# Kernel optimization log

Hardware: AMD Instinct MI355X
Metric: run time of the kernel (lower is better)

The kernel has to match this reference:

```python
import jax, jax.numpy as jnp
import numpy as np

ALPHA = 0.2  # LeakyReLU negative slope used throughout
NEG = -9e15


def _leaky(x, a=ALPHA):
    return jnp.where(x >= 0, x, a * x)


def _gat_layer(h, adj, W, a, concat):
    # h: [N, Fin], W: [Fin, Fout], a: [2*Fout, 1]
    Wh = h @ W                                   # [N, Fout]
    d = W.shape[-1]
    e = _leaky(Wh @ a[:d] + (Wh @ a[d:]).T)      # [N, N]
    att = jax.nn.softmax(jnp.where(adj > 0, e, NEG), axis=1)
    out = att @ Wh                               # [N, Fout]
    return jax.nn.elu(out) if concat else out


def setup_inputs() -> dict:
    key = jax.random.key(0)
    ks = jax.random.split(key, 24)
    N, F, H, D1, O1 = 4096, 512, 4, 256, 64
    x = jax.random.normal(ks[0], (N, F), dtype=jnp.float32)
    adj = jax.random.bernoulli(ks[1], 0.02, (N, N))
    adj = (adj | adj.T | jnp.eye(N, dtype=bool)).astype(jnp.float32)
    observation = jax.random.randint(ks[2], (1, N), 0, 2, dtype=jnp.int32)
    s_mat = jax.random.uniform(ks[3], (N, N), dtype=jnp.float32)
    theta = jax.random.uniform(ks[4], (1, F), dtype=jnp.float32)
    g = lambda k, s, sc: (jax.random.normal(k, s, dtype=jnp.float32) * sc)
    return {
        'x': x, 'adj': adj, 'observation': observation, 's_mat': s_mat,
        'theta': theta,
        'Wh0': g(ks[5], (H, F, D1), 0.05), 'ah0': g(ks[6], (H, 2 * D1, 1), 0.05),
        'Wh1': g(ks[7], (H, D1, D1), 0.05), 'ah1': g(ks[8], (H, 2 * D1, 1), 0.05),
        'Wo0': g(ks[9], (H * D1, O1), 0.05), 'ao0': g(ks[10], (2 * O1, 1), 0.05),
        'Wo1': g(ks[11], (O1, 1), 0.2), 'ao1': g(ks[12], (2, 1), 0.2),
        'dW': g(ks[13], (2, 10), 0.5), 'dW0': g(ks[14], (1, 10), 0.5),
        'dW1': g(ks[15], (10, 20), 0.5), 'dW01': g(ks[16], (1, 20), 0.5),
        'dW2': g(ks[17], (20, 10), 0.5), 'dW02': g(ks[18], (1, 10), 0.5),
        'dV': g(ks[19], (10, 1), 0.5), 'dV0': g(ks[20], (1, 1), 0.5),
    }


def reference(x, adj, observation, s_mat, theta, Wh0, ah0, Wh1, ah1,
              Wo0, ao0, Wo1, ao1, dW, dW0, dW1, dW01, dW2, dW02, dV, dV0):
    # mergeState: add theta to rows in the seed set (observation[0] == 1)
    seed = (observation[0] == 1).astype(x.dtype)[:, None]  # [N,1]
    h_in = x + seed * theta

    # multi-head 2-layer attention stacks (concat=True -> elu inside)
    def head(W0, a0, W1, a1):
        h = _gat_layer(h_in, adj, W0, a0, True)
        return _gat_layer(h, adj, W1, a1, True)

    hh = jax.vmap(head)(Wh0, ah0, Wh1, ah1)                 # [H, N, D1]
    hcat = jnp.transpose(hh, (1, 0, 2)).reshape(h_in.shape[0], -1)  # [N, H*D1]

    # output attention stack (concat=False), then elu (GAT.forward)
    h = _gat_layer(hcat, adj, Wo0, ao0, False)
    h = _gat_layer(h, adj, Wo1, ao1, False)
    h_ = jax.nn.elu(h)                                      # [N, 1]

    # GAT_degree v2: degreeNN over [h_, degree]
    d_v = s_mat.sum(axis=1, keepdims=True)                  # [N, 1]
    x_ = jnp.concatenate([h_, d_v], axis=1)                 # [N, 2]
    h0 = _leaky(x_ @ dW + dW0)
    h1 = _leaky(h0 @ dW1 + dW01)
    h2 = _leaky(h1 @ dW2 + dW02)
    return _leaky(h2 @ dV + dV0)                            # [N, 1]
```

## Files before the change

### kernel.cpp

```cpp
#include <hip/hip_runtime.h>
#include <hip/hip_bf16.h>
#include <hip/hip_fp16.h>
#include <math.h>

#define MAXDEG 512

typedef short v8s __attribute__((ext_vector_type(8)));
typedef float v4f __attribute__((ext_vector_type(4)));
typedef _Float16 h2 __attribute__((ext_vector_type(2)));

__device__ __forceinline__ float blockReduceSum(float v) {
    __shared__ float sh[8];
    int lane = threadIdx.x & 63, w = threadIdx.x >> 6;
    for (int o = 32; o > 0; o >>= 1) v += __shfl_down(v, o);
    __syncthreads();
    if (lane == 0) sh[w] = v;
    __syncthreads();
    if (w == 0) {
        int nw = (blockDim.x + 63) >> 6;
        v = (lane < nw) ? sh[lane] : 0.f;
        for (int o = 4; o > 0; o >>= 1) v += __shfl_down(v, o);
        if (lane == 0) sh[0] = v;
    }
    __syncthreads();
    return sh[0];
}

__device__ __forceinline__ float blockReduceMax(float v) {
    __shared__ float sh[8];
    int lane = threadIdx.x & 63, w = threadIdx.x >> 6;
    for (int o = 32; o > 0; o >>= 1) v = fmaxf(v, __shfl_down(v, o));
    __syncthreads();
    if (lane == 0) sh[w] = v;
    __syncthreads();
    if (w == 0) {
        int nw = (blockDim.x + 63) >> 6;
        v = (lane < nw) ? sh[lane] : -3.4e38f;
        for (int o = 4; o > 0; o >>= 1) v = fmaxf(v, __shfl_down(v, o));
        if (lane == 0) sh[0] = v;
    }
    __syncthreads();
    return sh[0];
}

__device__ __forceinline__ float leaky(float x) { return x >= 0.f ? x : 0.2f * x; }


__global__ void pre_small(const float* __restrict__ x, const int* __restrict__ obs,
                          const float* __restrict__ theta,
                          const float* __restrict__ Wh0, const float* __restrict__ Wh1,
                          const float* __restrict__ Wo0,
                          __half* __restrict__ hin, __half* __restrict__ Wh0t,
                          __half* __restrict__ Wh1t, __half* __restrict__ Wo0t,
                          float* __restrict__ elerZ, int elerN) {
    const int tid = threadIdx.x;
    int bb = blockIdx.x;
    if (bb < 1024) {
        int i8 = bb * 256 + tid;
        int n = i8 >> 6;
        int f = (i8 & 63) * 8;
        float4 a = *(const float4*)(x + (size_t)i8 * 8);
        float4 b = *(const float4*)(x + (size_t)i8 * 8 + 4);
        if (obs[n] == 1) {
            float4 ta = *(const float4*)(theta + f);
            float4 tb = *(const float4*)(theta + f + 4);
            a.x += ta.x; a.y += ta.y; a.z += ta.z; a.w += ta.w;
            b.x += tb.x; b.y += tb.y; b.z += tb.z; b.w += tb.w;
        }
        __half hv[8];
        hv[0] = __float2half(a.x); hv[1] = __float2half(a.y);
        hv[2] = __float2half(a.z); hv[3] = __float2half(a.w);
        hv[4] = __float2half(b.x); hv[5] = __float2half(b.y);
        hv[6] = __float2half(b.z); hv[7] = __float2half(b.w);
        *(uint4*)(hin + (size_t)i8 * 8) = *(const uint4*)hv;
        return;
    }
    bb -= 1024;
    if (bb < 72) {
        int i = bb * 256 + tid;
        *(float4*)(elerZ + (size_t)i * 4) = make_float4(0.f, 0.f, 0.f, 0.f);
        return;
    }
    int t = bb - 72;
    const float* src;
    __half* dst;
    int srcStride, dstStride;
    if (t < 128) {
        int b = t >> 5, tt = t & 31, kt = tt >> 2, mt = tt & 3;
        src = Wh0 + b * 131072 + (kt * 64) * 256 + mt * 64;
        dst = Wh0t + b * 131072 + (mt * 64) * 512 + kt * 64;
        srcStride = 256; dstStride = 512;
    } else if (t < 192) {
        int u = t - 128;
        int b = u >> 4, tt = u & 15, kt = tt >> 2, mt = tt & 3;
        src = Wh1 + b * 65536 + (kt * 64) * 256 + mt * 64;
        dst = Wh1t + b * 65536 + (mt * 64) * 256 + kt * 64;
        srcStride = 256; dstStride = 256;
    } else {
        int kt = t - 192;
        src = Wo0 + (kt * 64) * 64;
        dst = Wo0t + kt * 64;
        srcStride = 64; dstStride = 1024;
    }
    __shared__ float tile[64][65];
    int rr = tid >> 4;
    int cc = (tid & 15) * 4;
    #pragma unroll
    for (int sI = 0; sI < 4; sI++) {
        float4 v = *(const float4*)(src + (size_t)(rr + sI * 16) * srcStride + cc);
        tile[rr + sI * 16][cc]     = v.x;
        tile[rr + sI * 16][cc + 1] = v.y;
        tile[rr + sI * 16][cc + 2] = v.z;
        tile[rr + sI * 16][cc + 3] = v.w;
    }
    __syncthreads();
    int mr = tid >> 2;
    int kc = (tid & 3) * 16;
    #pragma unroll
    for (int g = 0; g < 2; g++) {
        v8s v;
        #pragma unroll
        for (int e = 0; e < 8; e++)
            v[e] = (short)__half_as_ushort(__float2half(tile[kc + g * 8 + e][mr]));
        *(v8s*)(dst + (size_t)mr * dstStride + kc + g * 8) = v;
    }
}

__global__ __launch_bounds__(256) void gemm1_csr(
    const __half* __restrict__ A, const __half* __restrict__ Bt,
    __half* __restrict__ C,
    const float* __restrict__ aVec, float* __restrict__ el, float* __restrict__ er,
    const float* __restrict__ adj, const float* __restrict__ s,
    int* __restrict__ colIdx, int* __restrict__ deg, float* __restrict__ dv,
    int N) {
    const int tid = threadIdx.x;
    if (blockIdx.x < 4096) {
        int row = blockIdx.x;
        __shared__ int cnt;
        if (tid == 0) cnt = 0;
        __syncthreads();
        const float4* ar = (const float4*)(adj + (size_t)row * N);
        const float4* sr = (const float4*)(s + (size_t)row * N);
        int* outp = colIdx + (size_t)row * MAXDEG;
        float psum = 0.f;
        const int n4 = N >> 2;
        for (int j4 = tid; j4 < n4; j4 += 256) {
            float4 a4 = ar[j4];
            float4 s4 = sr[j4];
            psum += (s4.x + s4.y) + (s4.z + s4.w);
            int jb = j4 << 2;
            if (a4.x > 0.f) { int p = atomicAdd(&cnt, 1); if (p < MAXDEG) outp[p] = jb; }
            if (a4.y > 0.f) { int p = atomicAdd(&cnt, 1); if (p < MAXDEG) outp[p] = jb + 1; }
            if (a4.z > 0.f) { int p = atomicAdd(&cnt, 1); if (p < MAXDEG) outp[p] = jb + 2; }
            if (a4.w > 0.f) { int p = atomicAdd(&cnt, 1); if (p < MAXDEG) outp[p] = jb + 3; }
        }
        psum = blockReduceSum(psum);
        __syncthreads();
        if (tid == 0) {
            deg[row] = cnt < MAXDEG ? cnt : MAXDEG;
            dv[row] = psum;
        }
        return;
    }
    const int g = blockIdx.x - 4096;
    const int bx = g & 1, by = (g >> 1) & 63, bz = g >> 7;
    const int K = 512, M = 256;
    const unsigned short* Ag = (const unsigned short*)A;
    const unsigned short* Bg = (const unsigned short*)Bt + (size_t)bz * 131072;
    __half* Cg = C + (size_t)bz * 4096 * 256;
    const float* av = aVec + (size_t)bz * 512;
    float* elb = el + (size_t)bz * 4096;
    float* erb = er + (size_t)bz * 4096;

    __shared__ __align__(16) unsigned short As[64][72];
    __shared__ __align__(16) unsigned short Bs[128][72];

    const int wave = tid >> 6, lane = tid & 63;
    const int wm = wave >> 1, wn = wave & 1;
    const int row0 = by * 64, col0 = bx * 128;
    const int lr = tid >> 2;
    const int lo = (tid & 3) * 16;
    const int m = lane & 15, quad = lane >> 4;

    v4f acc[2][4];
    #pragma unroll
    for (int i = 0; i < 2; i++)
        #pragma unroll
        for (int c = 0; c < 4; c++) acc[i][c] = (v4f)(0.f);

    for (int k0 = 0; k0 < K; k0 += 64) {
        *(int4*)(&As[lr][lo]) =
            *(const int4*)(Ag + (size_t)(row0 + lr) * K + k0 + lo);
        *(int4*)(&As[lr][lo + 8]) =
            *(const int4*)(Ag + (size_t)(row0 + lr) * K + k0 + lo + 8);
        *(int4*)(&Bs[lr][lo]) =
            *(const int4*)(Bg + (size_t)(col0 + lr) * K + k0 + lo);
        *(int4*)(&Bs[lr][lo + 8]) =
            *(const int4*)(Bg + (size_t)(col0 + lr) * K + k0 + lo + 8);
        *(int4*)(&Bs[lr + 64][lo]) =
            *(const int4*)(Bg + (size_t)(col0 + 64 + lr) * K + k0 + lo);
        *(int4*)(&Bs[lr + 64][lo + 8]) =
            *(const int4*)(Bg + (size_t)(col0 + 64 + lr) * K + k0 + lo + 8);
        __syncthreads();
        #pragma unroll
        for (int ks = 0; ks < 2; ks++) {
            v8s af[2], bfv[4];
            #pragma unroll
            for (int i = 0; i < 2; i++)
                af[i] = *(const v8s*)(&As[wm * 32 + i * 16 + m][ks * 32 + quad * 8]);
            #pragma unroll
            for (int c = 0; c < 4; c++)
                bfv[c] = *(const v8s*)(&Bs[wn * 64 + c * 16 + m][ks * 32 + quad * 8]);
            #pragma unroll
            for (int i = 0; i < 2; i++)
                #pragma unroll
                for (int c = 0; c < 4; c++)
                    acc[i][c] = __builtin_amdgcn_mfma_f32_16x16x32_f16(
                        af[i], bfv[c], acc[i][c], 0, 0, 0);
        }
        __syncthreads();
    }
    #pragma unroll
    for (int i = 0; i < 2; i++)
        #pragma unroll
        for (int c = 0; c < 4; c++)
            #pragma unroll
            for (int r = 0; r < 4; r++) {
                int row = row0 + wm * 32 + i * 16 + quad * 4 + r;
                int col = col0 + wn * 64 + c * 16 + m;
                Cg[(size_t)row * M + col] = __float2half(acc[i][c][r]);
            }
    float ael[4], aer[4];
    #pragma unroll
    for (int c = 0; c < 4; c++) {
        ael[c] = av[col0 + wn * 64 + c * 16 + m];
        aer[c] = av[M + col0 + wn * 64 + c * 16 + m];
    }
    #pragma unroll
    for (int i = 0; i < 2; i++)
        #pragma unroll
        for (int r = 0; r < 4; r++) {
            float pel = 0.f, per_ = 0.f;
            #pragma unroll
            for (int c = 0; c < 4; c++) {
                pel += acc[i][c][r] * ael[c];
                per_ += acc[i][c][r] * aer[c];
            }
            #pragma unroll
            for (int off = 1; off < 16; off <<= 1) {
                pel += __shfl_xor(pel, off);
                per_ += __shfl_xor(per_, off);
            }
            if (m == 0) {
                int row = row0 + wm * 32 + i * 16 + quad * 4 + r;
                atomicAdd(&elb[row], pel);
                atomicAdd(&erb[row], per_);
            }
        }
}

__global__ __launch_bounds__(256) void gemm_mfma64x128(
    const __half* __restrict__ A, const __half* __restrict__ Bt,
    __half* __restrict__ C, int N, int K, int M,
    size_t sA, size_t sB, size_t sC,
    const float* __restrict__ aVec, size_t aStride,
    float* __restrict__ el, float* __restrict__ er) {
    int b = blockIdx.z;
    const unsigned short* Ag = (const unsigned short*)(A + (size_t)b * sA);
    const unsigned short* Bg = (const unsigned short*)(Bt + (size_t)b * sB);
    __half* Cg = C + (size_t)b * sC;
    const float* av = aVec + (size_t)b * aStride;

    __shared__ __align__(16) unsigned short As[64][72];
    __shared__ __align__(16) unsigned short Bs[128][72];

    const int tid = threadIdx.x;
    const int wave = tid >> 6, lane = tid & 63;
    const int wm = wave >> 1, wn = wave & 1;
    const int row0 = blockIdx.y * 64, col0 = blockIdx.x * 128;
    const int lr = tid >> 2;
    const int lo = (tid & 3) * 16;
    const int m = lane & 15, quad = lane >> 4;

    v4f acc[2][4];
    #pragma unroll
    for (int i = 0; i < 2; i++)
        #pragma unroll
        for (int c = 0; c < 4; c++) acc[i][c] = (v4f)(0.f);

    for (int k0 = 0; k0 < K; k0 += 64) {
        *(int4*)(&As[lr][lo]) =
            *(const int4*)(Ag + (size_t)(row0 + lr) * K + k0 + lo);
        *(int4*)(&As[lr][lo + 8]) =
            *(const int4*)(Ag + (size_t)(row0 + lr) * K + k0 + lo + 8);
        *(int4*)(&Bs[lr][lo]) =
            *(const int4*)(Bg + (size_t)(col0 + lr) * K + k0 + lo);
        *(int4*)(&Bs[lr][lo + 8]) =
            *(const int4*)(Bg + (size_t)(col0 + lr) * K + k0 + lo + 8);
        *(int4*)(&Bs[lr + 64][lo]) =
            *(const int4*)(Bg + (size_t)(col0 + 64 + lr) * K + k0 + lo);
        *(int4*)(&Bs[lr + 64][lo + 8]) =
            *(const int4*)(Bg + (size_t)(col0 + 64 + lr) * K + k0 + lo + 8);
        __syncthreads();
        #pragma unroll
        for (int ks = 0; ks < 2; ks++) {
            v8s af[2], bfv[4];
            #pragma unroll
            for (int i = 0; i < 2; i++)
                af[i] = *(const v8s*)(&As[wm * 32 + i * 16 + m][ks * 32 + quad * 8]);
            #pragma unroll
            for (int c = 0; c < 4; c++)
                bfv[c] = *(const v8s*)(&Bs[wn * 64 + c * 16 + m][ks * 32 + quad * 8]);
            #pragma unroll
            for (int i = 0; i < 2; i++)
                #pragma unroll
                for (int c = 0; c < 4; c++)
                    acc[i][c] = __builtin_amdgcn_mfma_f32_16x16x32_f16(
                        af[i], bfv[c], acc[i][c], 0, 0, 0);
        }
        __syncthreads();
    }
    #pragma unroll
    for (int i = 0; i < 2; i++)
        #pragma unroll
        for (int c = 0; c < 4; c++)
            #pragma unroll
            for (int r = 0; r < 4; r++) {
                int row = row0 + wm * 32 + i * 16 + quad * 4 + r;
                int col = col0 + wn * 64 + c * 16 + m;
                Cg[(size_t)row * M + col] = __float2half(acc[i][c][r]);
            }
    float ael[4], aer[4];
    #pragma unroll
    for (int c = 0; c < 4; c++) {
        ael[c] = av[col0 + wn * 64 + c * 16 + m];
        aer[c] = av[M + col0 + wn * 64 + c * 16 + m];
    }
    #pragma unroll
    for (int i = 0; i < 2; i++)
        #pragma unroll
        for (int r = 0; r < 4; r++) {
            float pel = 0.f, per_ = 0.f;
            #pragma unroll
            for (int c = 0; c < 4; c++) {
                pel += acc[i][c][r] * ael[c];
                per_ += acc[i][c][r] * aer[c];
            }
            #pragma unroll
            for (int off = 1; off < 16; off <<= 1) {
                pel += __shfl_xor(pel, off);
                per_ += __shfl_xor(per_, off);
            }
            if (m == 0) {
                int row = row0 + wm * 32 + i * 16 + quad * 4 + r;
                atomicAdd(&el[(size_t)b * N + row], pel);
                atomicAdd(&er[(size_t)b * N + row], per_);
            }
        }
}

__global__ __launch_bounds__(256) void gemm_mfma16(
    const __half* __restrict__ A, const __half* __restrict__ Bt,
    __half* __restrict__ C, int N, int K, int M,
    const float* __restrict__ aVec,
    float* __restrict__ el, float* __restrict__ er) {
    const unsigned short* Ag = (const unsigned short*)A;
    const unsigned short* Bg = (const unsigned short*)Bt;
    __half* Cg = C;
    const float* av = aVec;

    __shared__ __align__(16) unsigned short As[16][72];
    __shared__ __align__(16) unsigned short Bs[64][72];

    const int tid = threadIdx.x;
    const int wave = tid >> 6, lane = tid & 63;
    const int row0 = blockIdx.y * 16;
    const int m = lane & 15, quad = lane >> 4;

    v4f acc = (v4f)(0.f);

    for (int k0 = 0; k0 < K; k0 += 64) {
        if (tid < 128) {
            int ar = tid >> 3, ac = (tid & 7) * 8;
            *(int4*)(&As[ar][ac]) =
                *(const int4*)(Ag + (size_t)(row0 + ar) * K + k0 + ac);
        }
        {
            int br = tid >> 2, bc = (tid & 3) * 16;
            *(int4*)(&Bs[br][bc]) =
                *(const int4*)(Bg + (size_t)br * K + k0 + bc);
            *(int4*)(&Bs[br][bc + 8]) =
                *(const int4*)(Bg + (size_t)br * K + k0 + bc + 8);
        }
        __syncthreads();
        #pragma unroll
        for (int ks = 0; ks < 2; ks++) {
            v8s af = *(const v8s*)(&As[m][ks * 32 + quad * 8]);
            v8s bf = *(const v8s*)(&Bs[wave * 16 + m][ks * 32 + quad * 8]);
            acc = __builtin_amdgcn_mfma_f32_16x16x32_f16(af, bf, acc, 0, 0, 0);
        }
        __syncthreads();
    }
    #pragma unroll
    for (int r = 0; r < 4; r++) {
        int row = row0 + quad * 4 + r;
        int col = wave * 16 + m;
        Cg[(size_t)row * M + col] = __float2half(acc[r]);
    }
    float ael = av[wave * 16 + m];
    float aer = av[M + wave * 16 + m];
    #pragma unroll
    for (int r = 0; r < 4; r++) {
        float pel = acc[r] * ael;
        float per_ = acc[r] * aer;
        #pragma unroll
        for (int off = 1; off < 16; off <<= 1) {
            pel += __shfl_xor(pel, off);
            per_ += __shfl_xor(per_, off);
        }
        if (m == 0) {
            int row = row0 + quad * 4 + r;
            atomicAdd(&el[row], pel);
            atomicAdd(&er[row], per_);
        }
    }
}

template<int D, int ACT, int HEADS, int FUSE>
__global__ __launch_bounds__(128) void attn_vec(
    const __half* __restrict__ Wh, const float* __restrict__ el,
    const float* __restrict__ er, const int* __restrict__ colIdx,
    const int* __restrict__ deg, __half* __restrict__ out,
    int N, size_t sWh, size_t sOut, int outRowStride,
    const float* __restrict__ wo1, const float* __restrict__ ao1,
    float* __restrict__ o2wh, float* __restrict__ el4, float* __restrict__ er4) {
    constexpr int LPN = D / 8;
    constexpr int SUBS = 64 / LPN;
    constexpr int PER_WAVE = SUBS * 4;
    constexpr int STEP = PER_WAVE * 2;

    const int tid = threadIdx.x;
    const int wave = tid >> 6, lane = tid & 63;
    int b, row;
    if (HEADS == 4) {
        int xcd = blockIdx.x & 7;
        b = xcd >> 1;
        row = ((xcd & 1) << 11) + ((blockIdx.x >> 3) << 1) + wave;
    } else {
        b = 0;
        row = blockIdx.x * 2 + wave;
    }

    const __half* whb = Wh + (size_t)b * sWh;
    const float* erb = er + (size_t)b * N;
    const float eln = el[(size_t)b * N + row];
    const int dc = deg[row];
    const int dcp = (dc + STEP - 1) & ~(STEP - 1);
    const int* ci = colIdx + (size_t)row * MAXDEG;

    __shared__ __align__(16) float2 spc[2][MAXDEG];
    float2* sp = spc[wave];

    float sreg[8];
    int jreg[8];
    float mx = -3.4e38f;
    #pragma unroll
    for (int s8 = 0; s8 < 8; s8++) {
        int k = s8 * 64 + lane;
        if (k < dc) {
            int j = ci[k];
            float s = eln + erb[j];
            s = fmaxf(s, 0.2f * s);
            sreg[s8] = s;
            jreg[s8] = j * (D * 2);
            mx = fmaxf(mx, s);
        }
    }
    #pragma unroll
    for (int off = 1; off < 64; off <<= 1) mx = fmaxf(mx, __shfl_xor(mx, off));

    float l = 0.f;
    #pragma unroll
    for (int s8 = 0; s8 < 8; s8++) {
        int k = s8 * 64 + lane;
        if (k < dc) {
            float p = __expf(sreg[s8] - mx);
            l += p;
            unsigned int pu = __half_as_ushort(__float2half(p));
            sp[k] = make_float2(__int_as_float(pu | (pu << 16)),
                                __int_as_float(jreg[s8]));
        }
    }
    for (int k = dc + lane; k < dcp; k += 64)
        sp[k] = make_float2(__int_as_float(0), __int_as_float(0));
    #pragma unroll
    for (int off = 1; off < 64; off <<= 1) l += __shfl_xor(l, off);
    const float inv = 1.f / l;

    asm volatile("s_waitcnt lgkmcnt(0)" ::: "memory");

    const int sub = lane / LPN;
    const int dl = (lane % LPN) * 8;
    const char* wp = (const char*)(whb + dl);

    union HU { unsigned int u; h2 h; };
    union R4 { uint4 u; h2 h[4]; };

    h2 a0[4], a1[4], a2[4], a3[4];
    #pragma unroll
    for (int i = 0; i < 4; i++) {
        a0[i] = (h2)(_Float16)0; a1[i] = (h2)(_Float16)0;
        a2[i] = (h2)(_Float16)0; a3[i] = (h2)(_Float16)0;
    }

    for (int k = sub * 4; k < dcp; k += STEP) {
        float4 pA = *(const float4*)(&sp[k]);
        float4 pB = *(const float4*)(&sp[k + 2]);
        float4 pC = *(const float4*)(&sp[k + PER_WAVE]);
        float4 pD = *(const float4*)(&sp[k + PER_WAVE + 2]);
        R4 r0, r1, r2, r3, r4, r5, r6, r7;
        r0.u = *(const uint4*)(wp + __float_as_int(pA.y));
        r1.u = *(const uint4*)(wp + __float_as_int(pA.w));
        r2.u = *(const uint4*)(wp + __float_as_int(pB.y));
        r3.u = *(const uint4*)(wp + __float_as_int(pB.w));
        r4.u = *(const uint4*)(wp + __float_as_int(pC.y));
        r5.u = *(const uint4*)(wp + __float_as_int(pC.w));
        r6.u = *(const uint4*)(wp + __float_as_int(pD.y));
        r7.u = *(const uint4*)(wp + __float_as_int(pD.w));
        HU p0, p1, p2, p3, p4, p5, p6, p7;
        p0.u = __float_as_int(pA.x);
        p1.u = __float_as_int(pA.z);
        p2.u = __float_as_int(pB.x);
        p3.u = __float_as_int(pB.z);
        p4.u = __float_as_int(pC.x);
        p5.u = __float_as_int(pC.z);
        p6.u = __float_as_int(pD.x);
        p7.u = __float_as_int(pD.z);
        #pragma unroll
        for (int i = 0; i < 4; i++) {
            a0[i] += p0.h * r0.h[i];
            a1[i] += p2.h * r2.h[i];
            a2[i] += p4.h * r4.h[i];
            a3[i] += p6.h * r6.h[i];
        }
        #pragma unroll
        for (int i = 0; i < 4; i++) {
            a0[i] += p1.h * r1.h[i];
            a1[i] += p3.h * r3.h[i];
            a2[i] += p5.h * r5.h[i];
            a3[i] += p7.h * r7.h[i];
        }
    }
    #pragma unroll
    for (int i = 0; i < 4; i++) a0[i] += (a1[i] + (a2[i] + a3[i]));
    #pragma unroll
    for (int off = LPN; off < 64; off <<= 1)
        #pragma unroll
        for (int i = 0; i < 4; i++) {
            HU t, s;
            t.h = a0[i];
            s.u = __shfl_xor((int)t.u, off);
            a0[i] += s.h;
        }

    if (FUSE) {
        if (sub == 0) {
            float t = 0.f;
            #pragma unroll
            for (int i = 0; i < 4; i++) {
                t += (float)a0[i][0] * inv * wo1[dl + 2 * i];
                t += (float)a0[i][1] * inv * wo1[dl + 2 * i + 1];
            }
            #pragma unroll
            for (int off = 1; off < LPN; off <<= 1) t += __shfl_xor(t, off);
            if (lane == 0) {
                o2wh[row] = t;
                el4[row] = t * ao1[0];
                er4[row] = t * ao1[1];
            }
        }
        return;
    }
    if (sub == 0) {
        __half hv[8];
        #pragma unroll
        for (int i = 0; i < 4; i++) {
            float v0 = (float)a0[i][0] * inv;
            float v1 = (float)a0[i][1] * inv;
            if (ACT == 1) {
                v0 = (v0 > 0.f) ? v0 : expm1f(v0);
                v1 = (v1 > 0.f) ? v1 : expm1f(v1);
            }
            hv[2 * i]     = __float2half(v0);
            hv[2 * i + 1] = __float2half(v1);
        }
        *(uint4*)(out + (size_t)b * sOut + (size_t)row * outRowStride + dl) =
            *(const uint4*)hv;
    }
}

__global__ void attn_d1_deg(const float* __restrict__ o2wh, const float* __restrict__ el,
                            const float* __restrict__ er, const int* __restrict__ colIdx,
                            const int* __restrict__ deg, const float* __restrict__ dv,
                            const float* __restrict__ dW, const float* __restrict__ dW0,
                            const float* __restrict__ dW1, const float* __restrict__ dW01,
                            const float* __restrict__ dW2, const float* __restrict__ dW02,
                            const float* __restrict__ dV, const float* __restrict__ dV0,
                            float* __restrict__ out, int N) {
    int row = blockIdx.x, tid = threadIdx.x;
    const float eln = el[row];
    const int dc = deg[row];
    const int* ci = colIdx + (size_t)row * MAXDEG;
    __shared__ float sp[MAXDEG];
    __shared__ int sc[MAXDEG];
    float mx = -3.4e38f;
    for (int k = tid; k < dc; k += blockDim.x) {
        int j = ci[k];
        sc[k] = j;
        float s = eln + er[j];
        s = fmaxf(s, 0.2f * s);
        sp[k] = s;
        mx = fmaxf(mx, s);
    }
    mx = blockReduceMax(mx);
    float l = 0.f, acc = 0.f;
    for (int k = tid; k < dc; k += blockDim.x) {
        float p = __expf(sp[k] - mx);
        l += p;
        acc += p * o2wh[sc[k]];
    }
    l = blockReduceSum(l);
    acc = blockReduceSum(acc);
    if (tid == 0) {
        float h = acc / l;
        h = (h > 0.f) ? h : expm1f(h);
        float d = dv[row];
        float t0[10], t1[20], t2[10];
        #pragma unroll
        for (int i = 0; i < 10; i++)
            t0[i] = leaky(h * dW[i] + d * dW[10 + i] + dW0[i]);
        #pragma unroll
        for (int j = 0; j < 20; j++) {
            float s = dW01[j];
            #pragma unroll
            for (int i = 0; i < 10; i++) s += t0[i] * dW1[i * 20 + j];
            t1[j] = leaky(s);
        }
        #pragma unroll
        for (int j = 0; j < 10; j++) {
            float s = dW02[j];
            #pragma unroll
            for (int i = 0; i < 20; i++) s += t1[i] * dW2[i * 10 + j];
            t2[j] = leaky(s);
        }
        float o = dV0[0];
        #pragma unroll
        for (int i = 0; i < 10; i++) o += t2[i] * dV[i];
        out[row] = leaky(o);
    }
}

extern "C" void kernel_launch(void* const* d_in, const int* in_sizes, int n_in,
                              void* d_out, int out_size, void* d_ws, size_t ws_size,
                              hipStream_t stream) {
    const int N = 4096, F = 512, H = 4, D1 = 256, O1 = 64;
    const float* x     = (const float*)d_in[0];
    const float* adj   = (const float*)d_in[1];
    const int*   obs   = (const int*)  d_in[2];
    const float* s_mat = (const float*)d_in[3];
    const float* theta = (const float*)d_in[4];
    const float* Wh0   = (const float*)d_in[5];
    const float* ah0   = (const float*)d_in[6];
    const float* Wh1   = (const float*)d_in[7];
    const float* ah1   = (const float*)d_in[8];
    const float* Wo0   = (const float*)d_in[9];
    const float* ao0   = (const float*)d_in[10];
    const float* Wo1   = (const float*)d_in[11];
    const float* ao1   = (const float*)d_in[12];
    const float* dWp   = (const float*)d_in[13];
    const float* dW0p  = (const float*)d_in[14];
    const float* dW1p  = (const float*)d_in[15];
    const float* dW01p = (const float*)d_in[16];
    const float* dW2p  = (const float*)d_in[17];
    const float* dW02p = (const float*)d_in[18];
    const float* dVp   = (const float*)d_in[19];
    const float* dV0p  = (const float*)d_in[20];
    float* outp = (float*)d_out;

    char* ws = (char*)d_ws;
    auto alloc = [&](size_t bytes) {
        char* p = ws;
        ws += (bytes + 255) & ~(size_t)255;
        return p;
    };
    __half* hin  = (__half*)alloc((size_t)N * F * 2);
    __half* whA  = (__half*)alloc((size_t)H * N * D1 * 2);
    __half* hb   = (__half*)alloc((size_t)H * N * D1 * 2);
    __half* hcat = (__half*)alloc((size_t)N * H * D1 * 2);
    __half* o1Wh = (__half*)alloc((size_t)N * O1 * 2);
    float* o2Wh  = (float*)alloc((size_t)N * 4);
    __half* Wh0t = (__half*)alloc((size_t)H * F * D1 * 2);
    __half* Wh1t = (__half*)alloc((size_t)H * D1 * D1 * 2);
    __half* Wo0t = (__half*)alloc((size_t)H * D1 * O1 * 2);
    int elerN = 4 * H * N + 2 * N;
    float* elerZ = (float*)alloc((size_t)elerN * 4);
    float* el1 = elerZ;
    float* er1 = el1 + H * N;
    float* el2 = er1 + H * N;
    float* er2 = el2 + H * N;
    float* el3 = er2 + H * N;
    float* er3 = el3 + N;
    float* el4 = (float*)alloc((size_t)N * 4);
    float* er4 = (float*)alloc((size_t)N * 4);
    float* dv  = (float*)alloc((size_t)N * 4);
    int* colIdx = (int*)alloc((size_t)N * MAXDEG * 4);
    int* deg    = (int*)alloc((size_t)N * 4);

    pre_small<<<1024 + 72 + 208, 256, 0, stream>>>(
        x, obs, theta, Wh0, Wh1, Wo0, hin, Wh0t, Wh1t, Wo0t, elerZ, elerN);

    gemm1_csr<<<4096 + 512, 256, 0, stream>>>(
        hin, Wh0t, whA, ah0, el1, er1,
        adj, s_mat, colIdx, deg, dv, N);
    attn_vec<256, 1, 4, 0><<<(N * H) / 2, 128, 0, stream>>>(
        whA, el1, er1, colIdx, deg, hb,
        N, (size_t)N * D1, (size_t)N * D1, D1,
        nullptr, nullptr, nullptr, nullptr, nullptr);

    gemm_mfma64x128<<<dim3(D1 / 128, N / 64, H), 256, 0, stream>>>(
        hb, Wh1t, whA, N, D1, D1, (size_t)N * D1, (size_t)D1 * D1, (size_t)N * D1,
        ah1, (size_t)2 * D1, el2, er2);
    attn_vec<256, 1, 4, 0><<<(N * H) / 2, 128, 0, stream>>>(
        whA, el2, er2, colIdx, deg, hcat,
        N, (size_t)N * D1, (size_t)D1, H * D1,
        nullptr, nullptr, nullptr, nullptr, nullptr);

    gemm_mfma16<<<dim3(1, N / 16, 1), 256, 0, stream>>>(
        hcat, Wo0t, o1Wh, N, H * D1, O1,
        ao0, el3, er3);
    attn_vec<64, 0, 1, 1><<<N / 2, 128, 0, stream>>>(
        o1Wh, el3, er3, colIdx, deg, nullptr,
        N, 0, 0, O1,
        Wo1, ao1, o2Wh, el4, er4);

    attn_d1_deg<<<N, 256, 0, stream>>>(o2Wh, el4, er4, colIdx, deg, dv,
        dWp, dW0p, dW1p, dW01p, dW2p, dW02p, dVp, dV0p, outp, N);
}
```

Baseline: 385.4 us.

## Wave-aggregate CSR atomics, reorder fused blocks, shrink GEMM K-tile

The CSR-build branch now loads all four float4s of adj and s_mat up front. It compacts column indices with one ballot plus a single per-wave LDS atomicAdd instead of one atomic per nonzero, which cuts shared-memory atomic contention. GEMM blocks are moved to the low block indices so they are scheduled before the 4096 CSR rows. The GEMM K-tile is halved from 64 to 32 to reduce LDS footprint, which raises occupancy but doubles the number of syncs per K loop. The unrolled loads assume N equals 4096.

```diff
diff --git a/kernel.cpp b/kernel.cpp
--- a/kernel.cpp
+++ b/kernel.cpp
@@ -134,25 +134,43 @@
     int* __restrict__ colIdx, int* __restrict__ deg, float* __restrict__ dv,
     int N) {
     const int tid = threadIdx.x;
-    if (blockIdx.x < 4096) {
-        int row = blockIdx.x;
+    const int lane = tid & 63;
+    if (blockIdx.x >= 512) {
+        int row = blockIdx.x - 512;
         __shared__ int cnt;
         if (tid == 0) cnt = 0;
         __syncthreads();
         const float4* ar = (const float4*)(adj + (size_t)row * N);
         const float4* sr = (const float4*)(s + (size_t)row * N);
         int* outp = colIdx + (size_t)row * MAXDEG;
+        float4 aa[4], ss[4];
+        #pragma unroll
+        for (int it = 0; it < 4; it++) {
+            aa[it] = ar[tid + it * 256];
+            ss[it] = sr[tid + it * 256];
+        }
         float psum = 0.f;
-        const int n4 = N >> 2;
-        for (int j4 = tid; j4 < n4; j4 += 256) {
-            float4 a4 = ar[j4];
-            float4 s4 = sr[j4];
-            psum += (s4.x + s4.y) + (s4.z + s4.w);
-            int jb = j4 << 2;
-            if (a4.x > 0.f) { int p = atomicAdd(&cnt, 1); if (p < MAXDEG) outp[p] = jb; }
-            if (a4.y > 0.f) { int p = atomicAdd(&cnt, 1); if (p < MAXDEG) outp[p] = jb + 1; }
-            if (a4.z > 0.f) { int p = atomicAdd(&cnt, 1); if (p < MAXDEG) outp[p] = jb + 2; }
-            if (a4.w > 0.f) { int p = atomicAdd(&cnt, 1); if (p < MAXDEG) outp[p] = jb + 3; }
+        #pragma unroll
+        for (int it = 0; it < 4; it++)
+            psum += (ss[it].x + ss[it].y) + (ss[it].z + ss[it].w);
+        #pragma unroll
+        for (int it = 0; it < 4; it++) {
+            int jb = (tid + it * 256) << 2;
+            float vals[4] = {aa[it].x, aa[it].y, aa[it].z, aa[it].w};
+            #pragma unroll
+            for (int c = 0; c < 4; c++) {
+                bool hit = vals[c] > 0.f;
+                unsigned long long mb = __ballot(hit);
+                if (mb) {
+                    int base = 0;
+                    if (lane == 0) base = atomicAdd(&cnt, __popcll(mb));
+                    base = __shfl(base, 0);
+                    if (hit) {
+                        int p = base + __popcll(mb & ((1ull << lane) - 1ull));
+                        if (p < MAXDEG) outp[p] = jb + c;
+                    }
+                }
+            }
         }
         psum = blockReduceSum(psum);
         __syncthreads();
@@ -162,7 +180,7 @@
         }
         return;
     }
-    const int g = blockIdx.x - 4096;
+    const int g = blockIdx.x;
     const int bx = g & 1, by = (g >> 1) & 63, bz = g >> 7;
     const int K = 512, M = 256;
     const unsigned short* Ag = (const unsigned short*)A;
@@ -172,14 +190,14 @@
     float* elb = el + (size_t)bz * 4096;
     float* erb = er + (size_t)bz * 4096;
 
-    __shared__ __align__(16) unsigned short As[64][72];
-    __shared__ __align__(16) unsigned short Bs[128][72];
-
-    const int wave = tid >> 6, lane = tid & 63;
+    __shared__ __align__(16) unsigned short As[64][40];
+    __shared__ __align__(16) unsigned short Bs[128][40];
+
+    const int wave = tid >> 6;
     const int wm = wave >> 1, wn = wave & 1;
     const int row0 = by * 64, col0 = bx * 128;
     const int lr = tid >> 2;
-    const int lo = (tid & 3) * 16;
+    const int lo = (tid & 3) * 8;
     const int m = lane & 15, quad = lane >> 4;
 
     v4f acc[2][4];
@@ -188,36 +206,27 @@
         #pragma unroll
         for (int c = 0; c < 4; c++) acc[i][c] = (v4f)(0.f);
 
-    for (int k0 = 0; k0 < K; k0 += 64) {
+    for (int k0 = 0; k0 < K; k0 += 32) {
         *(int4*)(&As[lr][lo]) =
             *(const int4*)(Ag + (size_t)(row0 + lr) * K + k0 + lo);
-        *(int4*)(&As[lr][lo + 8]) =
-            *(const int4*)(Ag + (size_t)(row0 + lr) * K + k0 + lo + 8);
         *(int4*)(&Bs[lr][lo]) =
             *(const int4*)(Bg + (size_t)(col0 + lr) * K + k0 + lo);
-        *(int4*)(&Bs[lr][lo + 8]) =
-            *(const int4*)(Bg + (size_t)(col0 + lr) * K + k0 + lo + 8);
         *(int4*)(&Bs[lr + 64][lo]) =
             *(const int4*)(Bg + (size_t)(col0 + 64 + lr) * K + k0 + lo);
-        *(int4*)(&Bs[lr + 64][lo + 8]) =
-            *(const int4*)(Bg + (size_t)(col0 + 64 + lr) * K + k0 + lo + 8);
         __syncthreads();
-        #pragma unroll
-        for (int ks = 0; ks < 2; ks++) {
-            v8s af[2], bfv[4];
-            #pragma unroll
-            for (int i = 0; i < 2; i++)
-                af[i] = *(const v8s*)(&As[wm * 32 + i * 16 + m][ks * 32 + quad * 8]);
+        v8s af[2], bfv[4];
+        #pragma unroll
+        for (int i = 0; i < 2; i++)
+            af[i] = *(const v8s*)(&As[wm * 32 + i * 16 + m][quad * 8]);
+        #pragma unroll
+        for (int c = 0; c < 4; c++)
+            bfv[c] = *(const v8s*)(&Bs[wn * 64 + c * 16 + m][quad * 8]);
+        #pragma unroll
+        for (int i = 0; i < 2; i++)
             #pragma unroll
             for (int c = 0; c < 4; c++)
-                bfv[c] = *(const v8s*)(&Bs[wn * 64 + c * 16 + m][ks * 32 + quad * 8]);
-            #pragma unroll
-            for (int i = 0; i < 2; i++)
-                #pragma unroll
-                for (int c = 0; c < 4; c++)
-                    acc[i][c] = __builtin_amdgcn_mfma_f32_16x16x32_f16(
-                        af[i], bfv[c], acc[i][c], 0, 0, 0);
-        }
+                acc[i][c] = __builtin_amdgcn_mfma_f32_16x16x32_f16(
+                    af[i], bfv[c], acc[i][c], 0, 0, 0);
         __syncthreads();
     }
     #pragma unroll
@@ -719,7 +728,7 @@
     pre_small<<<1024 + 72 + 208, 256, 0, stream>>>(
         x, obs, theta, Wh0, Wh1, Wo0, hin, Wh0t, Wh1t, Wo0t, elerZ, elerN);
 
-    gemm1_csr<<<4096 + 512, 256, 0, stream>>>(
+    gemm1_csr<<<512 + 4096, 256, 0, stream>>>(
         hin, Wh0t, whA, ah0, el1, er1,
         adj, s_mat, colIdx, deg, dv, N);
     attn_vec<256, 1, 4, 0><<<(N * H) / 2, 128, 0, stream>>>(
```

Result: faster. 375.4 us (-2.6%).
